# Performance work log

Measured on AMD Instinct MI355X. Metric: run time of the kernel, lower is better.

Reference implementation:

```python
import jax, jax.numpy as jnp
import numpy as np

N = 32768      # nodes
E = 524288     # edges (before self loops)
HID = 128      # hid_dim
HEADS = 4      # GAT heads
C = HID        # per-head channels (out_channels)
NEG_SLOPE = 0.2
LN_EPS = 1e-5


def setup_inputs() -> dict:
    key = jax.random.key(0)
    ks = jax.random.split(key, 12)
    s = 1.0 / np.sqrt(HID)
    return {
        "x": jax.random.normal(ks[0], (N, HID), jnp.float32),
        "edge_index": jax.random.randint(ks[1], (2, E), 0, N, jnp.int64),
        "w1": jax.random.normal(ks[2], (HID, HID), jnp.float32) * s,
        "b1": jnp.zeros((HID,), jnp.float32),
        "w2": jax.random.normal(ks[3], (HID, HID), jnp.float32) * s,
        "b2": jnp.zeros((HID,), jnp.float32),
        "ln_g": jnp.ones((HID,), jnp.float32),
        "ln_b": jnp.zeros((HID,), jnp.float32),
        "w_lin": jax.random.normal(ks[4], (HID, HEADS * C), jnp.float32) * s,
        "att_src": jax.random.normal(ks[5], (HEADS, C), jnp.float32) * s,
        "att_dst": jax.random.normal(ks[6], (HEADS, C), jnp.float32) * s,
        "bias": jnp.zeros((C,), jnp.float32),
    }


def _layernorm(h, g, b):
    mu = h.mean(-1, keepdims=True)
    var = ((h - mu) ** 2).mean(-1, keepdims=True)
    return (h - mu) * jax.lax.rsqrt(var + LN_EPS) * g + b


def reference(x, edge_index, w1, b1, w2, b2, ln_g, ln_b, w_lin, att_src, att_dst, bias):
    # MLP: Linear-ReLU-Linear-ReLU-LayerNorm
    h = jax.nn.relu(x @ w1 + b1)
    h = jax.nn.relu(h @ w2 + b2)
    h = _layernorm(h, ln_g, ln_b)

    # GATConv (PyG defaults: add_self_loops=True, shared lin for src/dst)
    loops = jnp.arange(N, dtype=edge_index.dtype)
    src = jnp.concatenate([edge_index[0], loops])
    dst = jnp.concatenate([edge_index[1], loops])

    xh = (h @ w_lin).reshape(N, HEADS, C)          # [N, H, C]
    a_src = jnp.einsum("nhc,hc->nh", xh, att_src)  # [N, H]
    a_dst = jnp.einsum("nhc,hc->nh", xh, att_dst)

    e = jax.nn.leaky_relu(a_src[src] + a_dst[dst], NEG_SLOPE)  # [E2, H]
    # segment softmax over incoming edges of each dst node
    m = jax.ops.segment_max(e, dst, num_segments=N)
    m = jnp.where(jnp.isfinite(m), m, 0.0)
    ex = jnp.exp(e - jax.lax.stop_gradient(m)[dst])
    denom = jax.ops.segment_sum(ex, dst, num_segments=N)
    alpha = ex / (denom[dst] + 1e-16)              # [E2, H]

    msg = xh[src] * alpha[:, :, None]              # [E2, H, C]
    out = jax.ops.segment_sum(msg, dst, num_segments=N)  # [N, H, C]
    return out.mean(axis=1) + bias                 # concat=False -> head mean
```

## Files before the change

kernel.cpp:

```cpp
#include <hip/hip_runtime.h>
#include <cstdint>

#define NN 32768
#define EE 524288
#define E2T (EE + NN)
#define HID 128
#define LDSW 136

typedef __attribute__((ext_vector_type(8)))  short s16x8;
typedef __attribute__((ext_vector_type(16))) float f32x16;

union V16 { uint4 u; s16x8 s; };

__device__ __forceinline__ float lrelu(float v) { return v > 0.0f ? v : 0.2f * v; }

__device__ __forceinline__ unsigned short f2bf(float f) {
  unsigned int u = __float_as_uint(f);
  return (unsigned short)((u + 0x7fffu + ((u >> 16) & 1u)) >> 16);
}
__device__ __forceinline__ float bf2f(unsigned short h) {
  return __uint_as_float(((unsigned int)h) << 16);
}
#define BF_LO(u) __uint_as_float((u) << 16)
#define BF_HI(u) __uint_as_float((u) & 0xffff0000u)

__global__ void k_pack(const float* __restrict__ w1, const float* __restrict__ w2,
                       const float* __restrict__ wl,
                       unsigned short* __restrict__ phi, unsigned short* __restrict__ plo)
{
  int idx = blockIdx.x * 256 + threadIdx.x;
  int r  = idx & 7;
  int l  = (idx >> 3) & 63;
  int kb = (idx >> 9) & 7;
  int s  = idx >> 12;
  const float* m; int ld, n;
  if (s < 4)      { m = w1; ld = 128; n = 32 * s       + (l & 31); }
  else if (s < 8) { m = w2; ld = 128; n = 32 * (s - 4) + (l & 31); }
  else            { m = wl; ld = 512; n = 32 * (s - 8) + (l & 31); }
  int k = 16 * kb + 8 * (l >> 5) + r;
  float f = m[(size_t)k * ld + n];
  unsigned short hi = f2bf(f);
  unsigned short lo = f2bf(f - bf2f(hi));
  phi[idx] = hi;
  plo[idx] = lo;
}

__device__ __forceinline__ void mm_pass(int slot, int lane,
    const unsigned short* __restrict__ phi, const unsigned short* __restrict__ plo,
    const unsigned short* hi_ls, const unsigned short* lo_ls, float accv[16])
{
  f32x16 acc1 = {0,0,0,0,0,0,0,0,0,0,0,0,0,0,0,0};
  f32x16 acc2 = {0,0,0,0,0,0,0,0,0,0,0,0,0,0,0,0};
  const int arow = lane & 31;
  const int h5 = lane >> 5;
  #pragma unroll
  for (int kb = 0; kb < 8; ++kb) {
    V16 bh, bl, ah, al;
    size_t boff = ((size_t)(slot * 8 + kb) * 64 + lane) * 8;
    bh.u = *(const uint4*)&phi[boff];
    bl.u = *(const uint4*)&plo[boff];
    int aoff = arow * LDSW + 16 * kb + 8 * h5;
    ah.u = *(const uint4*)&hi_ls[aoff];
    al.u = *(const uint4*)&lo_ls[aoff];
    acc1 = __builtin_amdgcn_mfma_f32_32x32x16_bf16(ah.s, bh.s, acc1, 0, 0, 0);
    acc2 = __builtin_amdgcn_mfma_f32_32x32x16_bf16(al.s, bh.s, acc2, 0, 0, 0);
    acc2 = __builtin_amdgcn_mfma_f32_32x32x16_bf16(ah.s, bl.s, acc2, 0, 0, 0);
  }
  #pragma unroll
  for (int r = 0; r < 16; ++r) accv[r] = acc1[r] + acc2[r];
}

__global__ __launch_bounds__(256) void k_fused(
    const float* __restrict__ x, const float* __restrict__ b1,
    const float* __restrict__ b2, const float* __restrict__ ln_g,
    const float* __restrict__ ln_b, const unsigned short* __restrict__ phi,
    const unsigned short* __restrict__ plo, unsigned short* __restrict__ xh)
{
  __shared__ unsigned short hi_ls[32 * LDSW];
  __shared__ unsigned short lo_ls[32 * LDSW];
  const int t = threadIdx.x;
  const int lane = t & 63;
  const int cf = t >> 6;
  const int row0 = blockIdx.x * 32;
  const int h5 = lane >> 5;
  float acc[16];

  {
    const int r = t >> 3, seg = t & 7;
    const float* src = &x[(size_t)(row0 + r) * HID + seg * 16];
    #pragma unroll
    for (int i = 0; i < 4; ++i) {
      float4 v = *(const float4*)(src + 4 * i);
      int c = seg * 16 + 4 * i;
      ushort4 h, l;
      h.x = f2bf(v.x); l.x = f2bf(v.x - bf2f(h.x));
      h.y = f2bf(v.y); l.y = f2bf(v.y - bf2f(h.y));
      h.z = f2bf(v.z); l.z = f2bf(v.z - bf2f(h.z));
      h.w = f2bf(v.w); l.w = f2bf(v.w - bf2f(h.w));
      *(ushort4*)&hi_ls[r * LDSW + c] = h;
      *(ushort4*)&lo_ls[r * LDSW + c] = l;
    }
  }
  __syncthreads();

  mm_pass(cf, lane, phi, plo, hi_ls, lo_ls, acc);
  __syncthreads();
  {
    const int col = 32 * cf + (lane & 31);
    const float bv = b1[col];
    #pragma unroll
    for (int r = 0; r < 16; ++r) {
      int row = (r & 3) + 8 * (r >> 2) + 4 * h5;
      float v = fmaxf(acc[r] + bv, 0.0f);
      unsigned short h = f2bf(v);
      hi_ls[row * LDSW + col] = h;
      lo_ls[row * LDSW + col] = f2bf(v - bf2f(h));
    }
  }
  __syncthreads();

  mm_pass(4 + cf, lane, phi, plo, hi_ls, lo_ls, acc);
  __syncthreads();
  {
    const int col = 32 * cf + (lane & 31);
    const float bv = b2[col];
    #pragma unroll
    for (int r = 0; r < 16; ++r) {
      int row = (r & 3) + 8 * (r >> 2) + 4 * h5;
      float v = fmaxf(acc[r] + bv, 0.0f);
      unsigned short h = f2bf(v);
      hi_ls[row * LDSW + col] = h;
      lo_ls[row * LDSW + col] = f2bf(v - bf2f(h));
    }
  }
  __syncthreads();

  {
    float g0 = ln_g[2 * lane], g1 = ln_g[2 * lane + 1];
    float be0 = ln_b[2 * lane], be1 = ln_b[2 * lane + 1];
    for (int i = 0; i < 8; ++i) {
      int row = 8 * cf + i;
      unsigned int hp = *(const unsigned int*)&hi_ls[row * LDSW + 2 * lane];
      unsigned int lp = *(const unsigned int*)&lo_ls[row * LDSW + 2 * lane];
      float v0 = bf2f((unsigned short)(hp & 0xffffu)) + bf2f((unsigned short)(lp & 0xffffu));
      float v1 = bf2f((unsigned short)(hp >> 16))     + bf2f((unsigned short)(lp >> 16));
      float s = v0 + v1, q = v0 * v0 + v1 * v1;
      #pragma unroll
      for (int off = 1; off < 64; off <<= 1) {
        s += __shfl_xor(s, off);
        q += __shfl_xor(q, off);
      }
      float mu = s * (1.0f / 128.0f);
      float var = q * (1.0f / 128.0f) - mu * mu;
      float rs = rsqrtf(var + 1e-5f);
      float o0 = (v0 - mu) * rs * g0 + be0;
      float o1 = (v1 - mu) * rs * g1 + be1;
      unsigned short h0 = f2bf(o0), h1 = f2bf(o1);
      unsigned short q0 = f2bf(o0 - bf2f(h0)), q1 = f2bf(o1 - bf2f(h1));
      *(unsigned int*)&hi_ls[row * LDSW + 2 * lane] = (unsigned int)h0 | ((unsigned int)h1 << 16);
      *(unsigned int*)&lo_ls[row * LDSW + 2 * lane] = (unsigned int)q0 | ((unsigned int)q1 << 16);
    }
  }
  __syncthreads();

  for (int hd = 0; hd < 4; ++hd) {
    mm_pass(8 + 4 * hd + cf, lane, phi, plo, hi_ls, lo_ls, acc);
    const int colg = 128 * hd + 32 * cf + (lane & 31);
    #pragma unroll
    for (int r = 0; r < 16; ++r) {
      int row = (r & 3) + 8 * (r >> 2) + 4 * h5;
      xh[(size_t)(row0 + row) * 512 + colg] = f2bf(acc[r]);
    }
  }
}

__global__ __launch_bounds__(256) void k_att(
    const unsigned short* __restrict__ xh, const float* __restrict__ att_s,
    const float* __restrict__ att_d, float* __restrict__ a_src,
    float* __restrict__ a_dst)
{
  const int lane = threadIdx.x & 63;
  const int n = blockIdx.x * 4 + (threadIdx.x >> 6);
  uint4 xv = *(const uint4*)&xh[(size_t)n * 512 + 8 * lane];
  const int head = lane >> 4;
  const int cb = 8 * (lane & 15);
  float4 s1 = *(const float4*)&att_s[head * 128 + cb];
  float4 s2 = *(const float4*)&att_s[head * 128 + cb + 4];
  float4 d1 = *(const float4*)&att_d[head * 128 + cb];
  float4 d2 = *(const float4*)&att_d[head * 128 + cb + 4];
  float x0 = BF_LO(xv.x), x1 = BF_HI(xv.x), x2 = BF_LO(xv.y), x3 = BF_HI(xv.y);
  float x4 = BF_LO(xv.z), x5 = BF_HI(xv.z), x6 = BF_LO(xv.w), x7 = BF_HI(xv.w);
  float ps = x0*s1.x + x1*s1.y + x2*s1.z + x3*s1.w + x4*s2.x + x5*s2.y + x6*s2.z + x7*s2.w;
  float pd = x0*d1.x + x1*d1.y + x2*d1.z + x3*d1.w + x4*d2.x + x5*d2.y + x6*d2.z + x7*d2.w;
  #pragma unroll
  for (int off = 1; off < 16; off <<= 1) {
    ps += __shfl_xor(ps, off);
    pd += __shfl_xor(pd, off);
  }
  if ((lane & 15) == 0) {
    a_src[n * 4 + head] = ps;
    a_dst[n * 4 + head] = pd;
  }
}

__global__ void k_hist(const int* __restrict__ ei, int* __restrict__ count)
{
  int i = blockIdx.x * 256 + threadIdx.x;
  if (i >= E2T) return;
  int dst = (i < EE) ? ei[EE + i] : (i - EE);
  atomicAdd(&count[dst], 1);
}

__global__ __launch_bounds__(256) void k_scan(const int* __restrict__ count,
                                              int* __restrict__ offsets,
                                              int* __restrict__ cursor)
{
  __shared__ int wtot[4];
  const int t = threadIdx.x;
  const int base = t * (NN / 256);
  int s = 0;
  for (int k = 0; k < NN / 256; ++k) s += count[base + k];
  const int lane = t & 63, w = t >> 6;
  int v = s;
  #pragma unroll
  for (int off = 1; off < 64; off <<= 1) {
    int u = __shfl_up(v, off);
    if (lane >= off) v += u;
  }
  if (lane == 63) wtot[w] = v;
  __syncthreads();
  int wpre = 0;
  for (int i = 0; i < w; ++i) wpre += wtot[i];
  int run = v + wpre - s;
  for (int k = 0; k < NN / 256; ++k) {
    offsets[base + k] = run;
    cursor[base + k] = run;
    run += count[base + k];
  }
  if (t == 255) offsets[NN] = run;
}

__global__ void k_scatter(const int* __restrict__ ei, int* __restrict__ cursor,
                          int* __restrict__ srcs)
{
  int i = blockIdx.x * 256 + threadIdx.x;
  if (i >= E2T) return;
  int s, d;
  if (i < EE) { s = ei[i]; d = ei[EE + i]; }
  else        { s = i - EE; d = s; }
  int pos = atomicAdd(&cursor[d], 1);
  srcs[pos] = s;
}

__global__ __launch_bounds__(256) void k_gat(
    const unsigned short* __restrict__ xh, const float* __restrict__ a_src,
    const float* __restrict__ a_dst, const int* __restrict__ offsets,
    const int* __restrict__ srcs, const float* __restrict__ bias,
    float* __restrict__ out)
{
  __shared__ float ex_ls[4][64][4];
  __shared__ int src_ls[4][64];
  const int lane = threadIdx.x & 63;
  const int w = threadIdx.x >> 6;
  const int n = blockIdx.x * 4 + w;
  const float4 adn = *(const float4*)&a_dst[n * 4];
  const int beg = offsets[n];
  const int deg = offsets[n + 1] - beg;
  const int h1 = lane >> 4;

  float acc[8] = {0, 0, 0, 0, 0, 0, 0, 0};
  float d0 = 0, d1 = 0, d2 = 0, d3 = 0;

  for (int j0 = 0; j0 < deg; j0 += 64) {
    int j = j0 + lane;
    if (j < deg) {
      int s = srcs[beg + j];
      float4 as = *(const float4*)&a_src[s * 4];
      float x0 = __expf(lrelu(as.x + adn.x));
      float x1 = __expf(lrelu(as.y + adn.y));
      float x2 = __expf(lrelu(as.z + adn.z));
      float x3 = __expf(lrelu(as.w + adn.w));
      d0 += x0; d1 += x1; d2 += x2; d3 += x3;
      ex_ls[w][lane][0] = x0; ex_ls[w][lane][1] = x1;
      ex_ls[w][lane][2] = x2; ex_ls[w][lane][3] = x3;
      src_ls[w][lane] = s;
    }
    __builtin_amdgcn_wave_barrier();
    const int cnt = min(64, deg - j0);
    #pragma unroll 4
    for (int jj = 0; jj < cnt; ++jj) {
      int s = src_ls[w][jj];
      float e = ex_ls[w][jj][h1];
      uint4 xv = *(const uint4*)(xh + (size_t)s * 512 + 8 * lane);
      acc[0] = fmaf(e, BF_LO(xv.x), acc[0]);
      acc[1] = fmaf(e, BF_HI(xv.x), acc[1]);
      acc[2] = fmaf(e, BF_LO(xv.y), acc[2]);
      acc[3] = fmaf(e, BF_HI(xv.y), acc[3]);
      acc[4] = fmaf(e, BF_LO(xv.z), acc[4]);
      acc[5] = fmaf(e, BF_HI(xv.z), acc[5]);
      acc[6] = fmaf(e, BF_LO(xv.w), acc[6]);
      acc[7] = fmaf(e, BF_HI(xv.w), acc[7]);
    }
    __builtin_amdgcn_wave_barrier();
  }

  #pragma unroll
  for (int off = 1; off < 64; off <<= 1) {
    d0 += __shfl_xor(d0, off); d1 += __shfl_xor(d1, off);
    d2 += __shfl_xor(d2, off); d3 += __shfl_xor(d3, off);
  }
  float dh = (h1 & 2) ? ((h1 & 1) ? d3 : d2) : ((h1 & 1) ? d1 : d0);
  float inv = 1.0f / (dh + 1e-16f);
  #pragma unroll
  for (int m = 0; m < 8; ++m) {
    float r = acc[m] * inv;
    r += __shfl_xor(r, 16);
    r += __shfl_xor(r, 32);
    acc[m] = r;
  }
  if (lane < 16) {
    const int c0 = 8 * lane;
    float4 o1, o2;
    o1.x = 0.25f * acc[0] + bias[c0 + 0];
    o1.y = 0.25f * acc[1] + bias[c0 + 1];
    o1.z = 0.25f * acc[2] + bias[c0 + 2];
    o1.w = 0.25f * acc[3] + bias[c0 + 3];
    o2.x = 0.25f * acc[4] + bias[c0 + 4];
    o2.y = 0.25f * acc[5] + bias[c0 + 5];
    o2.z = 0.25f * acc[6] + bias[c0 + 6];
    o2.w = 0.25f * acc[7] + bias[c0 + 7];
    *(float4*)&out[(size_t)n * HID + c0]     = o1;
    *(float4*)&out[(size_t)n * HID + c0 + 4] = o2;
  }
}

extern "C" void kernel_launch(void* const* d_in, const int* in_sizes, int n_in,
                              void* d_out, int out_size, void* d_ws, size_t ws_size,
                              hipStream_t stream)
{
  const float* x     = (const float*)d_in[0];
  const int*   ei    = (const int*)  d_in[1];
  const float* w1    = (const float*)d_in[2];
  const float* b1    = (const float*)d_in[3];
  const float* w2    = (const float*)d_in[4];
  const float* b2    = (const float*)d_in[5];
  const float* ln_g  = (const float*)d_in[6];
  const float* ln_b  = (const float*)d_in[7];
  const float* w_lin = (const float*)d_in[8];
  const float* att_s = (const float*)d_in[9];
  const float* att_d = (const float*)d_in[10];
  const float* bias  = (const float*)d_in[11];
  float* out = (float*)d_out;

  char* ws = (char*)d_ws;
  size_t off = 0;
  auto alloc = [&](size_t bytes) -> char* {
    char* p = ws + off;
    off += (bytes + 255) & ~(size_t)255;
    return p;
  };
  unsigned short* xh  = (unsigned short*)alloc((size_t)NN * 512 * 2);
  unsigned short* phi = (unsigned short*)alloc(98304 * 2);
  unsigned short* plo = (unsigned short*)alloc(98304 * 2);
  float* a_src  = (float*)alloc((size_t)NN * 4 * 4);
  float* a_dst  = (float*)alloc((size_t)NN * 4 * 4);
  int* count    = (int*)alloc((size_t)NN * 4);
  int* offsets  = (int*)alloc((size_t)(NN + 1) * 4);
  int* cursor   = (int*)alloc((size_t)NN * 4);
  int* srcs     = (int*)alloc((size_t)E2T * 4);
  if (off > ws_size) return;

  hipMemsetAsync(count, 0, (size_t)NN * 4, stream);

  k_pack<<<384, 256, 0, stream>>>(w1, w2, w_lin, phi, plo);
  k_hist<<<(E2T + 255) / 256, 256, 0, stream>>>(ei, count);
  k_scan<<<1, 256, 0, stream>>>(count, offsets, cursor);
  k_fused<<<NN / 32, 256, 0, stream>>>(x, b1, b2, ln_g, ln_b, phi, plo, xh);
  k_scatter<<<(E2T + 255) / 256, 256, 0, stream>>>(ei, cursor, srcs);
  k_att<<<NN / 4, 256, 0, stream>>>(xh, att_s, att_d, a_src, a_dst);
  k_gat<<<NN / 4, 256, 0, stream>>>(xh, a_src, a_dst, offsets, srcs, bias, out);
}
```

Baseline: 203.7 us.

## Slice xh by channel groups and split GAT aggregation across eight slice blocks

Stores the projected features as eight channel slices (node, head, 16 channels) and launches eight aggregation blocks per node group, each gathering from one slice with eight edges processed per wave step. This aims to shrink the per-block gather working set for better cache reuse and more parallelism. In exchange, softmax weights and edge lists are recomputed eight times and extra cross-lane reductions are added.

```diff
diff --git a/kernel.cpp b/kernel.cpp
--- a/kernel.cpp
+++ b/kernel.cpp
@@ -6,6 +6,7 @@
 #define E2T (EE + NN)
 #define HID 128
 #define LDSW 136
+#define SLICE_U16 2097152
 
 typedef __attribute__((ext_vector_type(8)))  short s16x8;
 typedef __attribute__((ext_vector_type(16))) float f32x16;
@@ -165,11 +166,13 @@
 
   for (int hd = 0; hd < 4; ++hd) {
     mm_pass(8 + 4 * hd + cf, lane, phi, plo, hi_ls, lo_ls, acc);
-    const int colg = 128 * hd + 32 * cf + (lane & 31);
+    const int col = 32 * cf + (lane & 31);
+    const int q = col >> 4, cin = col & 15;
+    unsigned short* base = xh + (size_t)q * SLICE_U16 + hd * 16 + cin;
     #pragma unroll
     for (int r = 0; r < 16; ++r) {
       int row = (r & 3) + 8 * (r >> 2) + 4 * h5;
-      xh[(size_t)(row0 + row) * 512 + colg] = f2bf(acc[r]);
+      base[(size_t)(row0 + row) * 64] = f2bf(acc[r]);
     }
   }
 }
@@ -181,13 +184,14 @@
 {
   const int lane = threadIdx.x & 63;
   const int n = blockIdx.x * 4 + (threadIdx.x >> 6);
-  uint4 xv = *(const uint4*)&xh[(size_t)n * 512 + 8 * lane];
   const int head = lane >> 4;
-  const int cb = 8 * (lane & 15);
-  float4 s1 = *(const float4*)&att_s[head * 128 + cb];
-  float4 s2 = *(const float4*)&att_s[head * 128 + cb + 4];
-  float4 d1 = *(const float4*)&att_d[head * 128 + cb];
-  float4 d2 = *(const float4*)&att_d[head * 128 + cb + 4];
+  const int c0 = 8 * (lane & 15);
+  const int q = c0 >> 4, cin = c0 & 15;
+  uint4 xv = *(const uint4*)&xh[(size_t)q * SLICE_U16 + (size_t)n * 64 + head * 16 + cin];
+  float4 s1 = *(const float4*)&att_s[head * 128 + c0];
+  float4 s2 = *(const float4*)&att_s[head * 128 + c0 + 4];
+  float4 d1 = *(const float4*)&att_d[head * 128 + c0];
+  float4 d2 = *(const float4*)&att_d[head * 128 + c0 + 4];
   float x0 = BF_LO(xv.x), x1 = BF_HI(xv.x), x2 = BF_LO(xv.y), x3 = BF_HI(xv.y);
   float x4 = BF_LO(xv.z), x5 = BF_HI(xv.z), x6 = BF_LO(xv.w), x7 = BF_HI(xv.w);
   float ps = x0*s1.x + x1*s1.y + x2*s1.z + x3*s1.w + x4*s2.x + x5*s2.y + x6*s2.z + x7*s2.w;
@@ -252,7 +256,7 @@
   srcs[pos] = s;
 }
 
-__global__ __launch_bounds__(256) void k_gat(
+__global__ __launch_bounds__(256) void k_gat2(
     const unsigned short* __restrict__ xh, const float* __restrict__ a_src,
     const float* __restrict__ a_dst, const int* __restrict__ offsets,
     const int* __restrict__ srcs, const float* __restrict__ bias,
@@ -262,44 +266,49 @@
   __shared__ int src_ls[4][64];
   const int lane = threadIdx.x & 63;
   const int w = threadIdx.x >> 6;
-  const int n = blockIdx.x * 4 + w;
+  const int q = blockIdx.x & 7;
+  const int n = (blockIdx.x >> 3) * 4 + w;
   const float4 adn = *(const float4*)&a_dst[n * 4];
   const int beg = offsets[n];
   const int deg = offsets[n + 1] - beg;
-  const int h1 = lane >> 4;
+  const int hsel = (lane & 7) >> 1;
+  const unsigned short* slice = xh + (size_t)q * SLICE_U16 + (lane & 7) * 8;
 
   float acc[8] = {0, 0, 0, 0, 0, 0, 0, 0};
   float d0 = 0, d1 = 0, d2 = 0, d3 = 0;
 
   for (int j0 = 0; j0 < deg; j0 += 64) {
     int j = j0 + lane;
+    float x0 = 0, x1 = 0, x2 = 0, x3 = 0;
+    int s = 0;
     if (j < deg) {
-      int s = srcs[beg + j];
+      s = __builtin_nontemporal_load(&srcs[beg + j]);
       float4 as = *(const float4*)&a_src[s * 4];
-      float x0 = __expf(lrelu(as.x + adn.x));
-      float x1 = __expf(lrelu(as.y + adn.y));
-      float x2 = __expf(lrelu(as.z + adn.z));
-      float x3 = __expf(lrelu(as.w + adn.w));
+      x0 = __expf(lrelu(as.x + adn.x));
+      x1 = __expf(lrelu(as.y + adn.y));
+      x2 = __expf(lrelu(as.z + adn.z));
+      x3 = __expf(lrelu(as.w + adn.w));
       d0 += x0; d1 += x1; d2 += x2; d3 += x3;
-      ex_ls[w][lane][0] = x0; ex_ls[w][lane][1] = x1;
-      ex_ls[w][lane][2] = x2; ex_ls[w][lane][3] = x3;
-      src_ls[w][lane] = s;
-    }
+    }
+    ex_ls[w][lane][0] = x0; ex_ls[w][lane][1] = x1;
+    ex_ls[w][lane][2] = x2; ex_ls[w][lane][3] = x3;
+    src_ls[w][lane] = s;
     __builtin_amdgcn_wave_barrier();
-    const int cnt = min(64, deg - j0);
+    const int cnt8 = (min(64, deg - j0) + 7) >> 3;
     #pragma unroll 4
-    for (int jj = 0; jj < cnt; ++jj) {
-      int s = src_ls[w][jj];
-      float e = ex_ls[w][jj][h1];
-      uint4 xv = *(const uint4*)(xh + (size_t)s * 512 + 8 * lane);
-      acc[0] = fmaf(e, BF_LO(xv.x), acc[0]);
-      acc[1] = fmaf(e, BF_HI(xv.x), acc[1]);
-      acc[2] = fmaf(e, BF_LO(xv.y), acc[2]);
-      acc[3] = fmaf(e, BF_HI(xv.y), acc[3]);
-      acc[4] = fmaf(e, BF_LO(xv.z), acc[4]);
-      acc[5] = fmaf(e, BF_HI(xv.z), acc[5]);
-      acc[6] = fmaf(e, BF_LO(xv.w), acc[6]);
-      acc[7] = fmaf(e, BF_HI(xv.w), acc[7]);
+    for (int g = 0; g < cnt8; ++g) {
+      int e = g * 8 + (lane >> 3);
+      float a = ex_ls[w][e][hsel];
+      int sv = src_ls[w][e];
+      uint4 xv = *(const uint4*)(slice + (size_t)sv * 64);
+      acc[0] = fmaf(a, BF_LO(xv.x), acc[0]);
+      acc[1] = fmaf(a, BF_HI(xv.x), acc[1]);
+      acc[2] = fmaf(a, BF_LO(xv.y), acc[2]);
+      acc[3] = fmaf(a, BF_HI(xv.y), acc[3]);
+      acc[4] = fmaf(a, BF_LO(xv.z), acc[4]);
+      acc[5] = fmaf(a, BF_HI(xv.z), acc[5]);
+      acc[6] = fmaf(a, BF_LO(xv.w), acc[6]);
+      acc[7] = fmaf(a, BF_HI(xv.w), acc[7]);
     }
     __builtin_amdgcn_wave_barrier();
   }
@@ -309,17 +318,20 @@
     d0 += __shfl_xor(d0, off); d1 += __shfl_xor(d1, off);
     d2 += __shfl_xor(d2, off); d3 += __shfl_xor(d3, off);
   }
-  float dh = (h1 & 2) ? ((h1 & 1) ? d3 : d2) : ((h1 & 1) ? d1 : d0);
-  float inv = 1.0f / (dh + 1e-16f);
+  float dsel = (hsel & 2) ? ((hsel & 1) ? d3 : d2) : ((hsel & 1) ? d1 : d0);
+  float inv = 1.0f / (dsel + 1e-16f);
   #pragma unroll
   for (int m = 0; m < 8; ++m) {
-    float r = acc[m] * inv;
-    r += __shfl_xor(r, 16);
-    r += __shfl_xor(r, 32);
-    acc[m] = r;
-  }
-  if (lane < 16) {
-    const int c0 = 8 * lane;
+    float v = acc[m] * inv;
+    v += __shfl_xor(v, 2);
+    v += __shfl_xor(v, 4);
+    v += __shfl_xor(v, 8);
+    v += __shfl_xor(v, 16);
+    v += __shfl_xor(v, 32);
+    acc[m] = v;
+  }
+  if (lane < 2) {
+    const int c0 = 16 * q + 8 * lane;
     float4 o1, o2;
     o1.x = 0.25f * acc[0] + bias[c0 + 0];
     o1.y = 0.25f * acc[1] + bias[c0 + 1];
@@ -359,7 +371,7 @@
     off += (bytes + 255) & ~(size_t)255;
     return p;
   };
-  unsigned short* xh  = (unsigned short*)alloc((size_t)NN * 512 * 2);
+  unsigned short* xh  = (unsigned short*)alloc((size_t)8 * SLICE_U16 * 2);
   unsigned short* phi = (unsigned short*)alloc(98304 * 2);
   unsigned short* plo = (unsigned short*)alloc(98304 * 2);
   float* a_src  = (float*)alloc((size_t)NN * 4 * 4);
@@ -378,5 +390,5 @@
   k_fused<<<NN / 32, 256, 0, stream>>>(x, b1, b2, ln_g, ln_b, phi, plo, xh);
   k_scatter<<<(E2T + 255) / 256, 256, 0, stream>>>(ei, cursor, srcs);
   k_att<<<NN / 4, 256, 0, stream>>>(xh, att_s, att_d, a_src, a_dst);
-  k_gat<<<NN / 4, 256, 0, stream>>>(xh, a_src, a_dst, offsets, srcs, bias, out);
-}
+  k_gat2<<<(NN / 4) * 8, 256, 0, stream>>>(xh, a_src, a_dst, offsets, srcs, bias, out);
+}
```

Result: slower. 328.8 us (+61.4%).
